# Kernel optimization log

Hardware: AMD Instinct MI355X
Metric: run time of the kernel (lower is better)

The kernel has to match this reference:

```python
import jax, jax.numpy as jnp
import numpy as np

N = 100000
E = 1600000
EPS = 1e-5
NEG_SLOPE = 0.01


def _leaky(x):
    return jnp.where(x > 0, x, NEG_SLOPE * x)


def _conv2d(x, w, b):
    # x: [N,Cin,H,W], w: [Cout,Cin,kh,kw], VALID padding, stride 1
    y = jax.lax.conv_general_dilated(x, w, (1, 1), 'VALID',
                                     dimension_numbers=('NCHW', 'OIHW', 'NCHW'))
    return y + b[None, :, None, None]


def _bn(x, g, b, m, v):
    # eval-mode BatchNorm1d over feature dim
    return (x - m) * (g / jnp.sqrt(v + EPS)) + b


def setup_inputs() -> dict:
    key = jax.random.key(0)
    ks = jax.random.split(key, 64)
    d = {}
    d['inputs'] = jax.random.normal(ks[0], (N, 1, 100, 5), dtype=jnp.float32)
    d['edge_index'] = jax.random.randint(ks[1], (2, E), 0, N, dtype=jnp.int32)
    # CNN encoder params (x=10)
    d['cw1'] = 0.1 * jax.random.normal(ks[2], (10, 1, 3, 3), dtype=jnp.float32)
    d['cb1'] = jnp.zeros((10,), jnp.float32)
    d['cw2'] = 0.1 * jax.random.normal(ks[3], (20, 10, 3, 2), dtype=jnp.float32)
    d['cb2'] = jnp.zeros((20,), jnp.float32)
    d['cw3'] = 0.1 * jax.random.normal(ks[4], (1, 20, 3, 2), dtype=jnp.float32)
    d['cb3'] = jnp.zeros((1,), jnp.float32)
    dims = [94, 128, 128, 64, 64, 16]
    for i in range(5):
        fi, fo = dims[i], dims[i + 1]
        k = 8 + 4 * i
        d[f'gw{i+1}'] = jax.random.normal(ks[k], (fi, fo), jnp.float32) / np.sqrt(fi)
        d[f'gb{i+1}'] = jnp.zeros((fo,), jnp.float32)
        d[f'bn{i+1}_g'] = 1.0 + 0.1 * jax.random.normal(ks[k + 1], (fo,), jnp.float32)
        d[f'bn{i+1}_b'] = 0.1 * jax.random.normal(ks[k + 2], (fo,), jnp.float32)
        d[f'bn{i+1}_m'] = 0.1 * jax.random.normal(ks[k + 3], (fo,), jnp.float32)
        d[f'bn{i+1}_v'] = jax.random.uniform(ks[k + 3], (fo,), jnp.float32, 0.5, 1.5)
    return d


def reference(inputs, edge_index,
              cw1, cb1, cw2, cb2, cw3, cb3,
              gw1, gb1, gw2, gb2, gw3, gb3, gw4, gb4, gw5, gb5,
              bn1_g, bn1_b, bn1_m, bn1_v,
              bn2_g, bn2_b, bn2_m, bn2_v,
              bn3_g, bn3_b, bn3_m, bn3_v,
              bn4_g, bn4_b, bn4_m, bn4_v,
              bn5_g, bn5_b, bn5_m, bn5_v):
    n = inputs.shape[0]
    # --- GCN normalization (self-loops + symmetric deg^-1/2) ---
    loops = jnp.arange(n, dtype=edge_index.dtype)
    src = jnp.concatenate([edge_index[0], loops])
    dst = jnp.concatenate([edge_index[1], loops])
    deg = jax.ops.segment_sum(jnp.ones_like(src, dtype=jnp.float32), dst, num_segments=n)
    dinv = jnp.where(deg > 0, jax.lax.rsqrt(deg), 0.0)
    norm = dinv[src] * dinv[dst]  # [E+N]

    def gcn(h, w, b):
        m = (h @ w)[src] * norm[:, None]
        return jax.ops.segment_sum(m, dst, num_segments=n) + b

    # --- CNN encoder (dropout identity in eval) ---
    h = _conv2d(inputs, cw1, cb1)
    h = _leaky(h)
    h = _conv2d(h, cw2, cb2)
    h = _leaky(h)
    h = _conv2d(h, cw3, cb3)  # [N,1,94,1]
    h = jnp.tanh(h.reshape(-1, 94))

    h = jnp.tanh(_bn(gcn(h, gw1, gb1), bn1_g, bn1_b, bn1_m, bn1_v))
    h = jnp.tanh(_bn(gcn(h, gw2, gb2), bn2_g, bn2_b, bn2_m, bn2_v))
    h = jnp.tanh(_bn(gcn(h, gw3, gb3), bn3_g, bn3_b, bn3_m, bn3_v))
    h = jnp.tanh(_bn(gcn(h, gw4, gb4), bn4_g, bn4_b, bn4_m, bn4_v))
    h = _bn(gcn(h, gw5, gb5), bn5_g, bn5_b, bn5_m, bn5_v)
    return jax.nn.softmax(h, axis=1)
```

## Files before the change

### kernel.cpp

```cpp
#include <hip/hip_runtime.h>
#include <math.h>

namespace {

constexpr int NN = 100000;
constexpr int NE = 1600000;
constexpr float EPS = 1e-5f;

__device__ __forceinline__ float leaky(float x) { return fmaxf(x, 0.01f * x); }
__device__ __forceinline__ float ffma(float a, float b, float c) { return __builtin_fmaf(a, b, c); }


__global__ __launch_bounds__(256) void k_init(int* __restrict__ deg, int* __restrict__ counter, int n) {
  int i = blockIdx.x * 256 + threadIdx.x;
  if (i < n) deg[i] = 1;
  if (i == 0) counter[0] = 0;
}

__global__ __launch_bounds__(256) void k_count(const int* __restrict__ dst, int* __restrict__ deg, int e) {
  int i = blockIdx.x * 256 + threadIdx.x;
  if (i < e) atomicAdd(&deg[dst[i]], 1);
}

__global__ __launch_bounds__(256) void k_alloc(const int* __restrict__ deg, float* __restrict__ dinv,
                                               int* __restrict__ offsets, int* __restrict__ cursor,
                                               int* __restrict__ counter, int n) {
  int i = blockIdx.x * 256 + threadIdx.x;
  int lane = threadIdx.x & 63;
  int c = 0;
  if (i < n) {
    int d = deg[i];
    dinv[i] = rsqrtf((float)d);
    c = d - 1;
  }
  int v = c;
#pragma unroll
  for (int s = 1; s < 64; s <<= 1) {
    int t = __shfl_up(v, s, 64);
    if (lane >= s) v += t;
  }
  int total = __shfl(v, 63, 64);
  int base = 0;
  if (lane == 63) base = atomicAdd(counter, total);
  base = __shfl(base, 63, 64);
  if (i < n) {
    int off = base + v - c;
    offsets[i] = off;
    cursor[i] = off;
  }
}

__global__ __launch_bounds__(256) void k_fill(const int* __restrict__ src, const int* __restrict__ dst,
                                              const float* __restrict__ dinv, int* __restrict__ cursor,
                                              int2* __restrict__ adj, int e) {
  int i = blockIdx.x * 256 + threadIdx.x;
  if (i < e) {
    int s = src[i], d = dst[i];
    int p = atomicAdd(&cursor[d], 1);
    adj[p] = make_int2(s, __float_as_int(dinv[s] * dinv[d]));
  }
}

__global__ __launch_bounds__(256) void k_padw1(const float* __restrict__ gw1, float* __restrict__ w1p) {
  int i = blockIdx.x * 256 + threadIdx.x;
  if (i < 96 * 128) w1p[i] = (i < 94 * 128) ? gw1[i] : 0.f;
}

struct BNParams {
  const float* bg[5];
  const float* bv[5];
  const float* gb[5];
  const float* bm[5];
  const float* bb[5];
};
__global__ __launch_bounds__(512) void k_bnprep(BNParams p, float* __restrict__ scale, float* __restrict__ shift) {
  int i = threadIdx.x;
  if (i >= 400) return;
  const int ends[5] = {128, 256, 320, 384, 400};
  int l = 0;
  while (i >= ends[l]) l++;
  int c = i - (l ? ends[l - 1] : 0);
  float sc = p.bg[l][c] * rsqrtf(p.bv[l][c] + EPS);
  scale[i] = sc;
  shift[i] = ffma(p.gb[l][c] - p.bm[l][c], sc, p.bb[l][c]);
}

__global__ __launch_bounds__(256, 4) void k_cnn(const float* __restrict__ x,
                                             const float* __restrict__ cw1, const float* __restrict__ cb1,
                                             const float* __restrict__ cw2, const float* __restrict__ cb2,
                                             const float* __restrict__ cw3, const float* __restrict__ cb3,
                                             float* __restrict__ H) {
  __shared__ __align__(16) float inb[2][500];
  __shared__ float c1[2][2940];
  __shared__ float part[2][2][2][98];

  int tid = threadIdx.x;
  int half = tid >> 7;
  int nt = tid & 127;
  int lane = tid & 63;
  int node = blockIdx.x * 2 + half;
  int co0 = __builtin_amdgcn_readfirstlane(((tid >> 6) & 1) * 10);

  for (int i = tid; i < 2 * 2 * 2 * 98; i += 256) ((float*)part)[i] = 0.f;

  if (nt < 125) {
    const float4* xp = (const float4*)(x + (size_t)node * 500);
    ((float4*)inb[half])[nt] = xp[nt];
  }
  __syncthreads();

  {
    const float* in = inb[half];
    float* c1p = c1[half];
    int h = nt;
    if (h < 98) {
      float xv[3][5];
#pragma unroll
      for (int kh = 0; kh < 3; kh++)
#pragma unroll
        for (int c = 0; c < 5; c++) xv[kh][c] = in[(h + kh) * 5 + c];
      float* rowp = c1p + h * 3;
#pragma unroll
      for (int co = 0; co < 10; co++) {
        float b = cb1[co];
        float a0 = b, a1 = b, a2 = b;
#pragma unroll
        for (int kh = 0; kh < 3; kh++)
#pragma unroll
          for (int kw = 0; kw < 3; kw++) {
            float wv = cw1[co * 9 + kh * 3 + kw];
            a0 = ffma(xv[kh][kw + 0], wv, a0);
            a1 = ffma(xv[kh][kw + 1], wv, a1);
            a2 = ffma(xv[kh][kw + 2], wv, a2);
          }
        rowp[co * 294 + 0] = leaky(a0);
        rowp[co * 294 + 1] = leaky(a1);
        rowp[co * 294 + 2] = leaky(a2);
      }
    }
  }
  __syncthreads();

  int hg = lane >> 1, w = lane & 1;
  int h0 = hg * 3;
  float acc[3][10];
#pragma unroll
  for (int a = 0; a < 3; a++)
#pragma unroll
    for (int c = 0; c < 10; c++) acc[a][c] = 0.f;
  {
    const float* c1p = c1[half];
#pragma unroll 1
    for (int ci = 0; ci < 10; ci++) {
      float r[5][2];
      const float* base = c1p + ci * 294 + h0 * 3 + w;
#pragma unroll
      for (int i = 0; i < 5; i++) {
        r[i][0] = base[i * 3];
        r[i][1] = base[i * 3 + 1];
      }
#pragma unroll
      for (int c = 0; c < 10; c++) {
        const float* wp = cw2 + (co0 + c) * 60 + ci * 6;
        float w0 = wp[0], w1 = wp[1], w2v = wp[2], w3v = wp[3], w4 = wp[4], w5 = wp[5];
#pragma unroll
        for (int hh = 0; hh < 3; hh++) {
          float t = acc[hh][c];
          t = ffma(r[hh][0],     w0,  t);
          t = ffma(r[hh][1],     w1,  t);
          t = ffma(r[hh + 1][0], w2v, t);
          t = ffma(r[hh + 1][1], w3v, t);
          t = ffma(r[hh + 2][0], w4,  t);
          t = ffma(r[hh + 2][1], w5,  t);
          acc[hh][c] = t;
        }
      }
    }
#pragma unroll
    for (int c = 0; c < 10; c++) {
      float b = cb2[co0 + c];
#pragma unroll
      for (int hh = 0; hh < 3; hh++) acc[hh][c] = leaky(acc[hh][c] + b);
    }
  }
  __syncthreads();

  {
    float* pp = &part[half][co0 == 0 ? 0 : 1][w][0];
#pragma unroll
    for (int kh = 0; kh < 3; kh++) {
      float ws[10];
#pragma unroll
      for (int c = 0; c < 10; c++) {
        float wa = cw3[(co0 + c) * 6 + kh * 2 + 0];
        float wb = cw3[(co0 + c) * 6 + kh * 2 + 1];
        ws[c] = w ? wb : wa;
      }
#pragma unroll
      for (int hh = 0; hh < 3; hh++) {
        float s = 0.f;
#pragma unroll
        for (int c = 0; c < 10; c++) s = ffma(acc[hh][c], ws[c], s);
        pp[h0 + hh - kh + 2] += s;
      }
      __syncthreads();
    }
  }

  {
    float* Hp = H + (size_t)node * 96;
    if (nt < 94) {
      float v = part[half][0][0][nt + 2] + part[half][0][1][nt + 2]
              + part[half][1][0][nt + 2] + part[half][1][1][nt + 2] + cb3[0];
      Hp[nt] = tanhf(v);
    } else if (nt < 96) {
      Hp[nt] = 0.f;
    }
  }
}

template <int K, int FO, int BN, bool EPI = false>
__global__ __launch_bounds__(256) void k_gemm(const float* __restrict__ A, const float* __restrict__ W,
                                              float* __restrict__ C, int M,
                                              const float* __restrict__ bns = nullptr,
                                              const float* __restrict__ bnh = nullptr,
                                              int bnofs = 0) {
  int tid = threadIdx.x;
  int row_base = blockIdx.x * 64;
  int col_base = blockIdx.y * BN;

  if constexpr (BN == 64) {
    __shared__ __align__(16) float As[K][68];
    __shared__ __align__(16) float Ws[K][BN];
    constexpr int K4 = K / 4;
    for (int idx = tid; idx < 64 * K4; idx += 256) {
      int r = idx / K4, kk = idx - r * K4;
      int row = row_base + r;
      float4 a = make_float4(0.f, 0.f, 0.f, 0.f);
      if (row < M) a = *(const float4*)&A[(size_t)row * K + kk * 4];
      As[kk * 4 + 0][r] = a.x;
      As[kk * 4 + 1][r] = a.y;
      As[kk * 4 + 2][r] = a.z;
      As[kk * 4 + 3][r] = a.w;
    }
    for (int idx = tid; idx < K * BN; idx += 256) {
      int r = idx / BN, c = idx - r * BN;
      Ws[r][c] = W[r * FO + col_base + c];
    }
    __syncthreads();

    int ty = tid >> 4, tx = tid & 15;
    float acc[4][4] = {};
#pragma unroll 4
    for (int k = 0; k < K; k++) {
      const float4 a = *(const float4*)&As[k][ty * 4];
      const float4 b = *(const float4*)&Ws[k][tx * 4];
      acc[0][0] = ffma(a.x, b.x, acc[0][0]); acc[0][1] = ffma(a.x, b.y, acc[0][1]);
      acc[0][2] = ffma(a.x, b.z, acc[0][2]); acc[0][3] = ffma(a.x, b.w, acc[0][3]);
      acc[1][0] = ffma(a.y, b.x, acc[1][0]); acc[1][1] = ffma(a.y, b.y, acc[1][1]);
      acc[1][2] = ffma(a.y, b.z, acc[1][2]); acc[1][3] = ffma(a.y, b.w, acc[1][3]);
      acc[2][0] = ffma(a.z, b.x, acc[2][0]); acc[2][1] = ffma(a.z, b.y, acc[2][1]);
      acc[2][2] = ffma(a.z, b.z, acc[2][2]); acc[2][3] = ffma(a.z, b.w, acc[2][3]);
      acc[3][0] = ffma(a.w, b.x, acc[3][0]); acc[3][1] = ffma(a.w, b.y, acc[3][1]);
      acc[3][2] = ffma(a.w, b.z, acc[3][2]); acc[3][3] = ffma(a.w, b.w, acc[3][3]);
    }
    float4 s4, h4;
    if constexpr (EPI) {
      s4 = *(const float4*)&bns[bnofs + col_base + tx * 4];
      h4 = *(const float4*)&bnh[bnofs + col_base + tx * 4];
    }
#pragma unroll
    for (int i = 0; i < 4; i++) {
      int row = row_base + ty * 4 + i;
      if (row < M) {
        float4 v;
        if constexpr (EPI) {
          v.x = tanhf(ffma(acc[i][0], s4.x, h4.x));
          v.y = tanhf(ffma(acc[i][1], s4.y, h4.y));
          v.z = tanhf(ffma(acc[i][2], s4.z, h4.z));
          v.w = tanhf(ffma(acc[i][3], s4.w, h4.w));
        } else {
          v = make_float4(acc[i][0], acc[i][1], acc[i][2], acc[i][3]);
        }
        *(float4*)&C[(size_t)row * FO + col_base + tx * 4] = v;
      }
    }
  } else {
    __shared__ float As[64][K + 1];
    __shared__ __align__(16) float Ws[K][BN];
    for (int idx = tid; idx < 64 * K; idx += 256) {
      int r = idx / K, k = idx - r * K;
      int row = row_base + r;
      As[r][k] = (row < M) ? A[(size_t)row * K + k] : 0.f;
    }
    for (int idx = tid; idx < K * BN; idx += 256) {
      int r = idx / BN, c = idx - r * BN;
      Ws[r][c] = W[r * FO + col_base + c];
    }
    __syncthreads();

    int ty = tid >> 2, tx = tid & 3;
    float acc[4] = {};
#pragma unroll 4
    for (int k = 0; k < K; k++) {
      float a = As[ty][k];
      const float4 b = *(const float4*)&Ws[k][tx * 4];
      acc[0] = ffma(a, b.x, acc[0]); acc[1] = ffma(a, b.y, acc[1]);
      acc[2] = ffma(a, b.z, acc[2]); acc[3] = ffma(a, b.w, acc[3]);
    }
    int row = row_base + ty;
    if (row < M) *(float4*)&C[(size_t)row * FO + col_base + tx * 4] = make_float4(acc[0], acc[1], acc[2], acc[3]);
  }
}

__global__ __launch_bounds__(256) void k_agg96(const float* __restrict__ Hm,
                                               const int* __restrict__ offsets, const int* __restrict__ deg,
                                               const int2* __restrict__ adj,
                                               const float* __restrict__ dinv,
                                               float* __restrict__ out, int n) {
  int tid = threadIdx.x;
  int li = tid >> 3, c12 = (tid & 7) * 12;
  int node = blockIdx.x * 32 + li;
  if (node >= n) return;

  float dv = dinv[node];
  float se = dv * dv;
  const float4* sp = (const float4*)&Hm[(size_t)node * 96 + c12];
  float4 a0 = sp[0], a1 = sp[1], a2 = sp[2];
  a0.x *= se; a0.y *= se; a0.z *= se; a0.w *= se;
  a1.x *= se; a1.y *= se; a1.z *= se; a1.w *= se;
  a2.x *= se; a2.y *= se; a2.z *= se; a2.w *= se;

  const int2* ap = adj + offsets[node];
  int cnt = deg[node] - 1;
  int e = 0;
  for (; e + 1 < cnt; e += 2) {
    int2 e0 = ap[e], e1 = ap[e + 1];
    float n0 = __int_as_float(e0.y), n1 = __int_as_float(e1.y);
    const float4* q0 = (const float4*)&Hm[(size_t)e0.x * 96 + c12];
    const float4* q1 = (const float4*)&Hm[(size_t)e1.x * 96 + c12];
    float4 u0 = q0[0], u1 = q0[1], u2 = q0[2];
    float4 v0 = q1[0], v1 = q1[1], v2 = q1[2];
    a0.x = ffma(u0.x, n0, a0.x); a0.y = ffma(u0.y, n0, a0.y);
    a0.z = ffma(u0.z, n0, a0.z); a0.w = ffma(u0.w, n0, a0.w);
    a1.x = ffma(u1.x, n0, a1.x); a1.y = ffma(u1.y, n0, a1.y);
    a1.z = ffma(u1.z, n0, a1.z); a1.w = ffma(u1.w, n0, a1.w);
    a2.x = ffma(u2.x, n0, a2.x); a2.y = ffma(u2.y, n0, a2.y);
    a2.z = ffma(u2.z, n0, a2.z); a2.w = ffma(u2.w, n0, a2.w);
    a0.x = ffma(v0.x, n1, a0.x); a0.y = ffma(v0.y, n1, a0.y);
    a0.z = ffma(v0.z, n1, a0.z); a0.w = ffma(v0.w, n1, a0.w);
    a1.x = ffma(v1.x, n1, a1.x); a1.y = ffma(v1.y, n1, a1.y);
    a1.z = ffma(v1.z, n1, a1.z); a1.w = ffma(v1.w, n1, a1.w);
    a2.x = ffma(v2.x, n1, a2.x); a2.y = ffma(v2.y, n1, a2.y);
    a2.z = ffma(v2.z, n1, a2.z); a2.w = ffma(v2.w, n1, a2.w);
  }
  if (e < cnt) {
    int2 e0 = ap[e];
    float n0 = __int_as_float(e0.y);
    const float4* q0 = (const float4*)&Hm[(size_t)e0.x * 96 + c12];
    float4 u0 = q0[0], u1 = q0[1], u2 = q0[2];
    a0.x = ffma(u0.x, n0, a0.x); a0.y = ffma(u0.y, n0, a0.y);
    a0.z = ffma(u0.z, n0, a0.z); a0.w = ffma(u0.w, n0, a0.w);
    a1.x = ffma(u1.x, n0, a1.x); a1.y = ffma(u1.y, n0, a1.y);
    a1.z = ffma(u1.z, n0, a1.z); a1.w = ffma(u1.w, n0, a1.w);
    a2.x = ffma(u2.x, n0, a2.x); a2.y = ffma(u2.y, n0, a2.y);
    a2.z = ffma(u2.z, n0, a2.z); a2.w = ffma(u2.w, n0, a2.w);
  }
  float4* op = (float4*)&out[(size_t)node * 96 + c12];
  op[0] = a0; op[1] = a1; op[2] = a2;
}

template <int FO, bool SOFT>
__global__ __launch_bounds__(256) void k_agg(const float* __restrict__ XW,
                                             const int* __restrict__ offsets, const int* __restrict__ deg,
                                             const int2* __restrict__ adj,
                                             const float* __restrict__ dinv,
                                             const float* __restrict__ bnscale, const float* __restrict__ bnshift,
                                             int bnofs, float* __restrict__ out, int n) {
  constexpr int TPN = FO / 8;
  constexpr int NPB = 256 / TPN;
  int tid = threadIdx.x;
  int li = tid / TPN, c8 = (tid % TPN) * 8;
  int node = blockIdx.x * NPB + li;
  if (node >= n) return;

  float dv = dinv[node];
  float se = dv * dv;
  const float4* selfp = (const float4*)&XW[(size_t)node * FO + c8];
  float4 aL = selfp[0], aH = selfp[1];
  aL.x *= se; aL.y *= se; aL.z *= se; aL.w *= se;
  aH.x *= se; aH.y *= se; aH.z *= se; aH.w *= se;

  const int2* ap = adj + offsets[node];
  int cnt = deg[node] - 1;
  int e = 0;
#define EDGE_STEP(AA)                                                        \
  {                                                                          \
    float nm = __int_as_float((AA).y);                                       \
    const float4* q = (const float4*)&XW[(size_t)(AA).x * FO + c8];          \
    float4 v = q[0], w = q[1];                                               \
    aL.x = ffma(v.x, nm, aL.x); aL.y = ffma(v.y, nm, aL.y);                  \
    aL.z = ffma(v.z, nm, aL.z); aL.w = ffma(v.w, nm, aL.w);                  \
    aH.x = ffma(w.x, nm, aH.x); aH.y = ffma(w.y, nm, aH.y);                  \
    aH.z = ffma(w.z, nm, aH.z); aH.w = ffma(w.w, nm, aH.w);                  \
  }
  for (; e + 3 < cnt; e += 4) {
    int2 a0 = ap[e], a1 = ap[e + 1], a2 = ap[e + 2], a3 = ap[e + 3];
    EDGE_STEP(a0); EDGE_STEP(a1); EDGE_STEP(a2); EDGE_STEP(a3);
  }
  for (; e < cnt; e++) {
    int2 a0 = ap[e];
    EDGE_STEP(a0);
  }
#undef EDGE_STEP

  const float4 s4L = *(const float4*)&bnscale[bnofs + c8];
  const float4 s4H = *(const float4*)&bnscale[bnofs + c8 + 4];
  const float4 h4L = *(const float4*)&bnshift[bnofs + c8];
  const float4 h4H = *(const float4*)&bnshift[bnofs + c8 + 4];
  float r[8];
  r[0] = ffma(aL.x, s4L.x, h4L.x); r[1] = ffma(aL.y, s4L.y, h4L.y);
  r[2] = ffma(aL.z, s4L.z, h4L.z); r[3] = ffma(aL.w, s4L.w, h4L.w);
  r[4] = ffma(aH.x, s4H.x, h4H.x); r[5] = ffma(aH.y, s4H.y, h4H.y);
  r[6] = ffma(aH.z, s4H.z, h4H.z); r[7] = ffma(aH.w, s4H.w, h4H.w);

  float4 oL, oH;
  if constexpr (SOFT) {
    float mx = r[0];
#pragma unroll
    for (int i = 1; i < 8; i++) mx = fmaxf(mx, r[i]);
#pragma unroll
    for (int m = TPN / 2; m; m >>= 1) mx = fmaxf(mx, __shfl_xor(mx, m, TPN));
    float sm = 0.f;
#pragma unroll
    for (int i = 0; i < 8; i++) { r[i] = expf(r[i] - mx); sm += r[i]; }
#pragma unroll
    for (int m = TPN / 2; m; m >>= 1) sm += __shfl_xor(sm, m, TPN);
    float inv = 1.f / sm;
#pragma unroll
    for (int i = 0; i < 8; i++) r[i] *= inv;
  } else {
#pragma unroll
    for (int i = 0; i < 8; i++) r[i] = tanhf(r[i]);
  }
  oL = make_float4(r[0], r[1], r[2], r[3]);
  oH = make_float4(r[4], r[5], r[6], r[7]);
  float4* op = (float4*)&out[(size_t)node * FO + c8];
  op[0] = oL;
  op[1] = oH;
}

}

extern "C" void kernel_launch(void* const* d_in, const int* in_sizes, int n_in,
                              void* d_out, int out_size, void* d_ws, size_t ws_size,
                              hipStream_t stream) {
  const float* x   = (const float*)d_in[0];
  const int*   ei  = (const int*)d_in[1];
  const float* cw1 = (const float*)d_in[2];
  const float* cb1 = (const float*)d_in[3];
  const float* cw2 = (const float*)d_in[4];
  const float* cb2 = (const float*)d_in[5];
  const float* cw3 = (const float*)d_in[6];
  const float* cb3 = (const float*)d_in[7];
  const float *gw[5], *gb[5], *bng[5], *bnb[5], *bnm[5], *bnv[5];
  for (int l = 0; l < 5; l++) {
    gw[l]  = (const float*)d_in[8 + 6 * l + 0];
    gb[l]  = (const float*)d_in[8 + 6 * l + 1];
    bng[l] = (const float*)d_in[8 + 6 * l + 2];
    bnb[l] = (const float*)d_in[8 + 6 * l + 3];
    bnm[l] = (const float*)d_in[8 + 6 * l + 4];
    bnv[l] = (const float*)d_in[8 + 6 * l + 5];
  }
  const int* srcp = ei;
  const int* dstp = ei + NE;

  char* w = (char*)d_ws;
  auto alloc = [&](size_t bytes) { char* p = w; w += (bytes + 255) & ~255ULL; return p; };
  int*   deg     = (int*)alloc((size_t)NN * 4);
  int*   offsets = (int*)alloc((size_t)NN * 4);
  int*   cursor  = (int*)alloc((size_t)NN * 4);
  int*   counter = (int*)alloc(256);
  float* dinv    = (float*)alloc((size_t)NN * 4);
  int2*  adj     = (int2*)alloc((size_t)NE * 8);
  float* w1p     = (float*)alloc(96 * 128 * 4);
  float* bnscale = (float*)alloc(400 * 4);
  float* bnshift = (float*)alloc(400 * 4);
  float* bufA    = (float*)alloc((size_t)NN * 128 * 4);
  float* bufB    = (float*)alloc((size_t)NN * 128 * 4);
  float* bufC    = (float*)alloc((size_t)NN * 128 * 4);

  int nb_n = (NN + 255) / 256;
  int nb_e = (NE + 255) / 256;
  k_init<<<nb_n, 256, 0, stream>>>(deg, counter, NN);
  k_count<<<nb_e, 256, 0, stream>>>(dstp, deg, NE);
  k_alloc<<<nb_n, 256, 0, stream>>>(deg, dinv, offsets, cursor, counter, NN);
  k_fill<<<nb_e, 256, 0, stream>>>(srcp, dstp, dinv, cursor, adj, NE);
  k_padw1<<<48, 256, 0, stream>>>(gw[0], w1p);
  {
    BNParams bp;
    for (int l = 0; l < 5; l++) {
      bp.bg[l] = bng[l]; bp.bv[l] = bnv[l]; bp.gb[l] = gb[l];
      bp.bm[l] = bnm[l]; bp.bb[l] = bnb[l];
    }
    k_bnprep<<<1, 512, 0, stream>>>(bp, bnscale, bnshift);
  }

  k_cnn<<<NN / 2, 256, 0, stream>>>(x, cw1, cb1, cw2, cb2, cw3, cb3, bufA);

  int gx = (NN + 63) / 64;
  k_agg96<<<(NN + 31) / 32, 256, 0, stream>>>(bufA, offsets, deg, adj, dinv, bufB, NN);
  k_gemm<96, 128, 64, true><<<dim3(gx, 2), 256, 0, stream>>>(bufB, w1p, bufC, NN, bnscale, bnshift, 0);
  k_gemm<128, 128, 64><<<dim3(gx, 2), 256, 0, stream>>>(bufC, gw[1], bufB, NN);
  k_agg<128, false><<<(NN + 15) / 16, 256, 0, stream>>>(bufB, offsets, deg, adj, dinv,
                                                        bnscale, bnshift, 128, bufA, NN);
  k_gemm<128, 64, 64><<<dim3(gx, 1), 256, 0, stream>>>(bufA, gw[2], bufB, NN);
  k_agg<64, false><<<(NN + 31) / 32, 256, 0, stream>>>(bufB, offsets, deg, adj, dinv,
                                                       bnscale, bnshift, 256, bufC, NN);
  k_gemm<64, 64, 64><<<dim3(gx, 1), 256, 0, stream>>>(bufC, gw[3], bufB, NN);
  k_agg<64, false><<<(NN + 31) / 32, 256, 0, stream>>>(bufB, offsets, deg, adj, dinv,
                                                       bnscale, bnshift, 320, bufA, NN);
  k_gemm<64, 16, 16><<<dim3(gx, 1), 256, 0, stream>>>(bufA, gw[4], bufB, NN);
  k_agg<16, true><<<(NN + 127) / 128, 256, 0, stream>>>(bufB, offsets, deg, adj, dinv,
                                                        bnscale, bnshift, 384, (float*)d_out, NN);
}
```

Before: 1.308 ms.

## Enlarge GEMM tiles to 128 rows with 8xN register blocking and split-K staging

Replaces the 64x64 tiled GEMM with a 128-row tile. Each thread now computes 8 rows by 4 or 8 columns, and the K dimension is staged through shared memory in two halves to bound LDS use. For the 128-wide layers one block covers all output columns, so A is loaded once rather than once per column tile. Weight loads are vectorized. The larger per-thread accumulator raises register pressure and the bigger tiles halve the grid, which may reduce occupancy.

Result: no change. 1.295 ms (-1.0%).

```diff
diff --git a/kernel.cpp b/kernel.cpp
--- a/kernel.cpp
+++ b/kernel.cpp
@@ -220,97 +220,130 @@
 }
 
 template <int K, int FO, int BN, bool EPI = false>
-__global__ __launch_bounds__(256) void k_gemm(const float* __restrict__ A, const float* __restrict__ W,
-                                              float* __restrict__ C, int M,
-                                              const float* __restrict__ bns = nullptr,
-                                              const float* __restrict__ bnh = nullptr,
-                                              int bnofs = 0) {
+__global__ __launch_bounds__(256) void k_gemm2(const float* __restrict__ A, const float* __restrict__ W,
+                                               float* __restrict__ C, int M,
+                                               const float* __restrict__ bns = nullptr,
+                                               const float* __restrict__ bnh = nullptr,
+                                               int bnofs = 0) {
+  constexpr int BM = 128;
+  constexpr int KT = K / 2;
+  constexpr int CPT = BN / 16;
+  __shared__ __align__(16) float As[KT][BM + 4];
+  __shared__ __align__(16) float Ws[KT][BN + 4];
   int tid = threadIdx.x;
-  int row_base = blockIdx.x * 64;
+  int row_base = blockIdx.x * BM;
   int col_base = blockIdx.y * BN;
-
-  if constexpr (BN == 64) {
-    __shared__ __align__(16) float As[K][68];
-    __shared__ __align__(16) float Ws[K][BN];
-    constexpr int K4 = K / 4;
-    for (int idx = tid; idx < 64 * K4; idx += 256) {
+  int ty = tid >> 4, tx = tid & 15;
+
+  float acc[8][CPT];
+#pragma unroll
+  for (int i = 0; i < 8; i++)
+#pragma unroll
+    for (int j = 0; j < CPT; j++) acc[i][j] = 0.f;
+
+#pragma unroll 1
+  for (int kh = 0; kh < 2; kh++) {
+    if (kh) __syncthreads();
+    constexpr int K4 = KT / 4;
+    for (int idx = tid; idx < BM * K4; idx += 256) {
       int r = idx / K4, kk = idx - r * K4;
       int row = row_base + r;
       float4 a = make_float4(0.f, 0.f, 0.f, 0.f);
-      if (row < M) a = *(const float4*)&A[(size_t)row * K + kk * 4];
+      if (row < M) a = *(const float4*)&A[(size_t)row * K + kh * KT + kk * 4];
       As[kk * 4 + 0][r] = a.x;
       As[kk * 4 + 1][r] = a.y;
       As[kk * 4 + 2][r] = a.z;
       As[kk * 4 + 3][r] = a.w;
     }
-    for (int idx = tid; idx < K * BN; idx += 256) {
-      int r = idx / BN, c = idx - r * BN;
-      Ws[r][c] = W[r * FO + col_base + c];
+    constexpr int B4 = BN / 4;
+    for (int idx = tid; idx < KT * B4; idx += 256) {
+      int r = idx / B4, c4 = idx - r * B4;
+      float4 wv = *(const float4*)&W[(size_t)(kh * KT + r) * FO + col_base + c4 * 4];
+      *(float4*)&Ws[r][c4 * 4] = wv;
     }
     __syncthreads();
 
-    int ty = tid >> 4, tx = tid & 15;
-    float acc[4][4] = {};
+#pragma unroll 2
+    for (int k = 0; k < KT; k++) {
+      const float4 a0 = *(const float4*)&As[k][ty * 8];
+      const float4 a1 = *(const float4*)&As[k][ty * 8 + 4];
+      float ar[8] = {a0.x, a0.y, a0.z, a0.w, a1.x, a1.y, a1.z, a1.w};
+      float bc[CPT];
+      {
+        const float4 b0 = *(const float4*)&Ws[k][tx * CPT];
+        bc[0] = b0.x; bc[1] = b0.y; bc[2] = b0.z; bc[3] = b0.w;
+        if constexpr (CPT == 8) {
+          const float4 b1 = *(const float4*)&Ws[k][tx * CPT + 4];
+          bc[4] = b1.x; bc[5] = b1.y; bc[6] = b1.z; bc[7] = b1.w;
+        }
+      }
+#pragma unroll
+      for (int i = 0; i < 8; i++)
+#pragma unroll
+        for (int j = 0; j < CPT; j++) acc[i][j] = ffma(ar[i], bc[j], acc[i][j]);
+    }
+  }
+
+  float s[CPT], h[CPT];
+  if constexpr (EPI) {
+    const float4 s0 = *(const float4*)&bns[bnofs + col_base + tx * CPT];
+    const float4 h0 = *(const float4*)&bnh[bnofs + col_base + tx * CPT];
+    s[0] = s0.x; s[1] = s0.y; s[2] = s0.z; s[3] = s0.w;
+    h[0] = h0.x; h[1] = h0.y; h[2] = h0.z; h[3] = h0.w;
+    if constexpr (CPT == 8) {
+      const float4 s1 = *(const float4*)&bns[bnofs + col_base + tx * CPT + 4];
+      const float4 h1 = *(const float4*)&bnh[bnofs + col_base + tx * CPT + 4];
+      s[4] = s1.x; s[5] = s1.y; s[6] = s1.z; s[7] = s1.w;
+      h[4] = h1.x; h[5] = h1.y; h[6] = h1.z; h[7] = h1.w;
+    }
+  }
+#pragma unroll
+  for (int i = 0; i < 8; i++) {
+    int row = row_base + ty * 8 + i;
+    if (row < M) {
+      float o[CPT];
+#pragma unroll
+      for (int j = 0; j < CPT; j++) {
+        if constexpr (EPI) o[j] = tanhf(ffma(acc[i][j], s[j], h[j]));
+        else               o[j] = acc[i][j];
+      }
+      float* cp = &C[(size_t)row * FO + col_base + tx * CPT];
+      *(float4*)cp = make_float4(o[0], o[1], o[2], o[3]);
+      if constexpr (CPT == 8) *(float4*)(cp + 4) = make_float4(o[4], o[5], o[6], o[7]);
+    }
+  }
+}
+
+__global__ __launch_bounds__(256) void k_gemm16(const float* __restrict__ A, const float* __restrict__ W,
+                                                float* __restrict__ C, int M) {
+  constexpr int K = 64, FO = 16;
+  __shared__ float As[64][K + 1];
+  __shared__ __align__(16) float Ws[K][FO];
+  int tid = threadIdx.x;
+  int row_base = blockIdx.x * 64;
+
+  for (int idx = tid; idx < 64 * K; idx += 256) {
+    int r = idx / K, k = idx - r * K;
+    int row = row_base + r;
+    As[r][k] = (row < M) ? A[(size_t)row * K + k] : 0.f;
+  }
+  for (int idx = tid; idx < K * FO; idx += 256) {
+    int r = idx / FO, c = idx - r * FO;
+    Ws[r][c] = W[r * FO + c];
+  }
+  __syncthreads();
+
+  int ty = tid >> 2, tx = tid & 3;
+  float acc[4] = {};
 #pragma unroll 4
-    for (int k = 0; k < K; k++) {
-      const float4 a = *(const float4*)&As[k][ty * 4];
-      const float4 b = *(const float4*)&Ws[k][tx * 4];
-      acc[0][0] = ffma(a.x, b.x, acc[0][0]); acc[0][1] = ffma(a.x, b.y, acc[0][1]);
-      acc[0][2] = ffma(a.x, b.z, acc[0][2]); acc[0][3] = ffma(a.x, b.w, acc[0][3]);
-      acc[1][0] = ffma(a.y, b.x, acc[1][0]); acc[1][1] = ffma(a.y, b.y, acc[1][1]);
-      acc[1][2] = ffma(a.y, b.z, acc[1][2]); acc[1][3] = ffma(a.y, b.w, acc[1][3]);
-      acc[2][0] = ffma(a.z, b.x, acc[2][0]); acc[2][1] = ffma(a.z, b.y, acc[2][1]);
-      acc[2][2] = ffma(a.z, b.z, acc[2][2]); acc[2][3] = ffma(a.z, b.w, acc[2][3]);
-      acc[3][0] = ffma(a.w, b.x, acc[3][0]); acc[3][1] = ffma(a.w, b.y, acc[3][1]);
-      acc[3][2] = ffma(a.w, b.z, acc[3][2]); acc[3][3] = ffma(a.w, b.w, acc[3][3]);
-    }
-    float4 s4, h4;
-    if constexpr (EPI) {
-      s4 = *(const float4*)&bns[bnofs + col_base + tx * 4];
-      h4 = *(const float4*)&bnh[bnofs + col_base + tx * 4];
-    }
-#pragma unroll
-    for (int i = 0; i < 4; i++) {
-      int row = row_base + ty * 4 + i;
-      if (row < M) {
-        float4 v;
-        if constexpr (EPI) {
-          v.x = tanhf(ffma(acc[i][0], s4.x, h4.x));
-          v.y = tanhf(ffma(acc[i][1], s4.y, h4.y));
-          v.z = tanhf(ffma(acc[i][2], s4.z, h4.z));
-          v.w = tanhf(ffma(acc[i][3], s4.w, h4.w));
-        } else {
-          v = make_float4(acc[i][0], acc[i][1], acc[i][2], acc[i][3]);
-        }
-        *(float4*)&C[(size_t)row * FO + col_base + tx * 4] = v;
-      }
-    }
-  } else {
-    __shared__ float As[64][K + 1];
-    __shared__ __align__(16) float Ws[K][BN];
-    for (int idx = tid; idx < 64 * K; idx += 256) {
-      int r = idx / K, k = idx - r * K;
-      int row = row_base + r;
-      As[r][k] = (row < M) ? A[(size_t)row * K + k] : 0.f;
-    }
-    for (int idx = tid; idx < K * BN; idx += 256) {
-      int r = idx / BN, c = idx - r * BN;
-      Ws[r][c] = W[r * FO + col_base + c];
-    }
-    __syncthreads();
-
-    int ty = tid >> 2, tx = tid & 3;
-    float acc[4] = {};
-#pragma unroll 4
-    for (int k = 0; k < K; k++) {
-      float a = As[ty][k];
-      const float4 b = *(const float4*)&Ws[k][tx * 4];
-      acc[0] = ffma(a, b.x, acc[0]); acc[1] = ffma(a, b.y, acc[1]);
-      acc[2] = ffma(a, b.z, acc[2]); acc[3] = ffma(a, b.w, acc[3]);
-    }
-    int row = row_base + ty;
-    if (row < M) *(float4*)&C[(size_t)row * FO + col_base + tx * 4] = make_float4(acc[0], acc[1], acc[2], acc[3]);
-  }
+  for (int k = 0; k < K; k++) {
+    float a = As[ty][k];
+    const float4 b = *(const float4*)&Ws[k][tx * 4];
+    acc[0] = ffma(a, b.x, acc[0]); acc[1] = ffma(a, b.y, acc[1]);
+    acc[2] = ffma(a, b.z, acc[2]); acc[3] = ffma(a, b.w, acc[3]);
+  }
+  int row = row_base + ty;
+  if (row < M) *(float4*)&C[(size_t)row * FO + tx * 4] = make_float4(acc[0], acc[1], acc[2], acc[3]);
 }
 
 __global__ __launch_bounds__(256) void k_agg96(const float* __restrict__ Hm,
@@ -508,19 +541,19 @@
 
   k_cnn<<<NN / 2, 256, 0, stream>>>(x, cw1, cb1, cw2, cb2, cw3, cb3, bufA);
 
-  int gx = (NN + 63) / 64;
+  int gx2 = (NN + 127) / 128;
   k_agg96<<<(NN + 31) / 32, 256, 0, stream>>>(bufA, offsets, deg, adj, dinv, bufB, NN);
-  k_gemm<96, 128, 64, true><<<dim3(gx, 2), 256, 0, stream>>>(bufB, w1p, bufC, NN, bnscale, bnshift, 0);
-  k_gemm<128, 128, 64><<<dim3(gx, 2), 256, 0, stream>>>(bufC, gw[1], bufB, NN);
+  k_gemm2<96, 128, 128, true><<<dim3(gx2, 1), 256, 0, stream>>>(bufB, w1p, bufC, NN, bnscale, bnshift, 0);
+  k_gemm2<128, 128, 128><<<dim3(gx2, 1), 256, 0, stream>>>(bufC, gw[1], bufB, NN);
   k_agg<128, false><<<(NN + 15) / 16, 256, 0, stream>>>(bufB, offsets, deg, adj, dinv,
                                                         bnscale, bnshift, 128, bufA, NN);
-  k_gemm<128, 64, 64><<<dim3(gx, 1), 256, 0, stream>>>(bufA, gw[2], bufB, NN);
+  k_gemm2<128, 64, 64><<<dim3(gx2, 1), 256, 0, stream>>>(bufA, gw[2], bufB, NN);
   k_agg<64, false><<<(NN + 31) / 32, 256, 0, stream>>>(bufB, offsets, deg, adj, dinv,
                                                        bnscale, bnshift, 256, bufC, NN);
-  k_gemm<64, 64, 64><<<dim3(gx, 1), 256, 0, stream>>>(bufC, gw[3], bufB, NN);
+  k_gemm2<64, 64, 64><<<dim3(gx2, 1), 256, 0, stream>>>(bufC, gw[3], bufB, NN);
   k_agg<64, false><<<(NN + 31) / 32, 256, 0, stream>>>(bufB, offsets, deg, adj, dinv,
                                                        bnscale, bnshift, 320, bufA, NN);
-  k_gemm<64, 16, 16><<<dim3(gx, 1), 256, 0, stream>>>(bufA, gw[4], bufB, NN);
+  k_gemm16<<<(NN + 63) / 64, 256, 0, stream>>>(bufA, gw[4], bufB, NN);
   k_agg<16, true><<<(NN + 127) / 128, 256, 0, stream>>>(bufB, offsets, deg, adj, dinv,
                                                         bnscale, bnshift, 384, (float*)d_out, NN);
 }
```
